# Performance work log

Hardware: AMD Instinct MI355X
Metric: run time of the kernel (lower is better)

Reference implementation:

```python
import jax, jax.numpy as jnp
import numpy as np

H = 16  # num_heads
LN_EPS = 1e-5


def _layernorm(x):
    # parameter-free LayerNorm over last dim (the source module creates no LN params)
    mu = jnp.mean(x, axis=-1, keepdims=True)
    var = jnp.var(x, axis=-1, keepdims=True)
    return (x - mu) / jnp.sqrt(var + LN_EPS)


def setup_inputs() -> dict:
    key = jax.random.key(0)
    B, L, D = 8, 1024, 1024
    ks = jax.random.split(key, 12)
    s = 1.0 / np.sqrt(D)
    s4 = 1.0 / np.sqrt(4 * D)
    return {
        "x": jax.random.normal(ks[0], (B, L, D), dtype=jnp.float32),
        "Wq": jax.random.normal(ks[1], (D, D), dtype=jnp.float32) * s,
        "bq": jnp.zeros((D,), dtype=jnp.float32),
        "Wk": jax.random.normal(ks[2], (D, D), dtype=jnp.float32) * s,
        "bk": jnp.zeros((D,), dtype=jnp.float32),
        "Wv": jax.random.normal(ks[3], (D, D), dtype=jnp.float32) * s,
        "bv": jnp.zeros((D,), dtype=jnp.float32),
        "W1": jax.random.normal(ks[4], (D, 4 * D), dtype=jnp.float32) * s,
        "b1": jnp.zeros((4 * D,), dtype=jnp.float32),
        "W2": jax.random.normal(ks[5], (4 * D, D), dtype=jnp.float32) * s4,
        "b2": jnp.zeros((D,), dtype=jnp.float32),
    }


def reference(x, Wq, bq, Wk, bk, Wv, bv, W1, b1, W2, b2):
    B, L, D = x.shape
    Dh = D // H

    def split(t):  # [B,L,D] -> [B,H,L,Dh]
        return t.reshape(B, L, H, Dh).transpose(0, 2, 1, 3)

    q = split(x @ Wq + bq)
    k = split(x @ Wk + bk)
    v = split(x @ Wv + bv)

    # naive full-score attention, materializes [B,H,L,L]
    score = jnp.einsum("bhld,bhmd->bhlm", q, k) / jnp.sqrt(jnp.float32(Dh))
    attn = jax.nn.softmax(score, axis=-1)
    out = jnp.einsum("bhlm,bhmd->bhld", attn, v)
    out = out.transpose(0, 2, 1, 3).reshape(B, L, D)  # concat heads

    x = _layernorm(x + out)  # dropout = identity (eval)
    ffn = jax.nn.gelu(x @ W1 + b1, approximate=False) @ W2 + b2
    x = _layernorm(x + ffn)
    return x
```

## Files before the change

### kernel.cpp

```cpp
#include <hip/hip_runtime.h>

typedef unsigned short u16;
typedef __attribute__((ext_vector_type(8))) short bf16x8;
typedef __attribute__((ext_vector_type(4))) float f32x4;

#define MFMA16(a, b, c) __builtin_amdgcn_mfma_f32_16x16x32_bf16(a, b, c, 0, 0, 0)

__device__ __forceinline__ float b2f(u16 u) {
    unsigned int x = ((unsigned int)u) << 16;
    return __builtin_bit_cast(float, x);
}
__device__ __forceinline__ u16 f2b(float f) {
    unsigned int u = __builtin_bit_cast(unsigned int, f);
    u = u + 0x7fffu + ((u >> 16) & 1u);
    return (u16)(u >> 16);
}
__device__ __forceinline__ float gelu_f(float x) {
    return 0.5f * x * (1.0f + erff(x * 0.70710678118654752f));
}
__device__ __forceinline__ void gload_lds16(const u16* g, u16* lds) {
    __builtin_amdgcn_global_load_lds(
        (const __attribute__((address_space(1))) unsigned int*)g,
        (__attribute__((address_space(3))) unsigned int*)lds, 16, 0, 0);
}

__global__ __launch_bounds__(256) void cvt_f2b_kernel(
    const float* __restrict__ in, u16* __restrict__ out, int n)
{
    const int i = (blockIdx.x * 256 + threadIdx.x) * 4;
    if (i >= n) return;
    float4 v = *(const float4*)&in[i];
    ushort4 o;
    o.x = f2b(v.x); o.y = f2b(v.y); o.z = f2b(v.z); o.w = f2b(v.w);
    *(ushort4*)&out[i] = o;
}

__global__ __launch_bounds__(256) void transpose_cvt(
    const float* __restrict__ in, u16* __restrict__ out, int R, int C)
{
    __shared__ u16 tile[64][65];
    const int t = threadIdx.x;
    const int r0 = blockIdx.y * 64, c0 = blockIdx.x * 64;
    const int tr = t >> 4, tc = (t & 15) * 4;
#pragma unroll
    for (int p = 0; p < 4; p++) {
        const int rr = tr + p * 16;
        float4 v = *(const float4*)&in[(size_t)(r0 + rr) * C + c0 + tc];
        tile[rr][tc + 0] = f2b(v.x); tile[rr][tc + 1] = f2b(v.y);
        tile[rr][tc + 2] = f2b(v.z); tile[rr][tc + 3] = f2b(v.w);
    }
    __syncthreads();
#pragma unroll
    for (int p = 0; p < 4; p++) {
        const int cc = tr + p * 16;
        ushort4 v;
        v.x = tile[tc + 0][cc]; v.y = tile[tc + 1][cc];
        v.z = tile[tc + 2][cc]; v.w = tile[tc + 3][cc];
        *(ushort4*)&out[(size_t)(c0 + cc) * R + r0 + tc] = v;
    }
}

template <int EPI>
__global__ __launch_bounds__(256, 2) void gemm_bt(
    const u16* __restrict__ A, const u16* __restrict__ Bt,
    const float* __restrict__ bias, u16* __restrict__ C,
    int M, int N, int K)
{
    __shared__ __attribute__((aligned(16))) u16 sA[2][128 * 32];
    __shared__ __attribute__((aligned(16))) u16 sB[2][128 * 32];
    const int t = threadIdx.x;
    const int lane = t & 63, w = t >> 6;
    const int g = lane >> 4, r = lane & 15;
    const int wr = w >> 1, wc = w & 1;
    const int m0 = blockIdx.y * 128, n0 = blockIdx.x * 128;
    const int arow0 = t >> 2;
    const int ake = (t & 3) * 8;
    const int ldsb = w * 512;

    const f32x4 fz = {0.f, 0.f, 0.f, 0.f};
    f32x4 acc[4][4];
#pragma unroll
    for (int i = 0; i < 4; i++)
#pragma unroll
        for (int j = 0; j < 4; j++) acc[i][j] = fz;

#pragma unroll
    for (int it = 0; it < 2; ++it) {
        gload_lds16(&A[(size_t)(m0 + arow0 + it * 64) * K + ake], &sA[0][ldsb + it * 2048]);
        gload_lds16(&Bt[(size_t)(n0 + arow0 + it * 64) * K + ake], &sB[0][ldsb + it * 2048]);
    }
    __syncthreads();

    const int nk = K >> 5;
    for (int kt = 0; kt < nk; ++kt) {
        const int buf = kt & 1;
        if (kt + 1 < nk) {
            const int k0 = (kt + 1) << 5;
#pragma unroll
            for (int it = 0; it < 2; ++it) {
                gload_lds16(&A[(size_t)(m0 + arow0 + it * 64) * K + k0 + ake], &sA[buf ^ 1][ldsb + it * 2048]);
                gload_lds16(&Bt[(size_t)(n0 + arow0 + it * 64) * K + k0 + ake], &sB[buf ^ 1][ldsb + it * 2048]);
            }
        }
        bf16x8 af[4], bfr[4];
#pragma unroll
        for (int i = 0; i < 4; i++)
            af[i] = *(const bf16x8*)&sA[buf][(wr * 64 + i * 16 + r) * 32 + g * 8];
#pragma unroll
        for (int j = 0; j < 4; j++)
            bfr[j] = *(const bf16x8*)&sB[buf][(wc * 64 + j * 16 + r) * 32 + g * 8];
#pragma unroll
        for (int i = 0; i < 4; i++)
#pragma unroll
            for (int j = 0; j < 4; j++)
                acc[i][j] = MFMA16(af[i], bfr[j], acc[i][j]);
        __syncthreads();
    }

#pragma unroll
    for (int i = 0; i < 4; i++) {
#pragma unroll
        for (int j = 0; j < 4; j++) {
            const int col = n0 + wc * 64 + j * 16 + r;
            const float bs = bias[col];
            const int row0 = m0 + wr * 64 + i * 16 + g * 4;
            if (EPI == 2) {
                const int brow = row0 >> 10;
                const int l = row0 & 1023;
                const int vrow = ((brow << 4) + (col >> 6)) * 64 + (col & 63);
                ushort4 pk;
                pk.x = f2b(acc[i][j][0] + bs);
                pk.y = f2b(acc[i][j][1] + bs);
                pk.z = f2b(acc[i][j][2] + bs);
                pk.w = f2b(acc[i][j][3] + bs);
                *(ushort4*)&C[(size_t)vrow * 1024 + l] = pk;
            } else {
#pragma unroll
                for (int rg = 0; rg < 4; ++rg) {
                    float v = acc[i][j][rg] + bs;
                    if (EPI == 1) v = gelu_f(v);
                    C[(size_t)(row0 + rg) * N + col] = f2b(v);
                }
            }
        }
    }
}

__global__ __launch_bounds__(256, 2) void attn_fwd(
    const u16* __restrict__ Q, const u16* __restrict__ Kb,
    const u16* __restrict__ Vt, u16* __restrict__ O)
{
    __shared__ __attribute__((aligned(16))) u16 sK[2][64 * 64];
    __shared__ __attribute__((aligned(16))) u16 sV[2][64 * 64];
    __shared__ __attribute__((aligned(16))) u16 sP[4][32 * 72];
    const int t = threadIdx.x;
    const int lane = t & 63, w = t >> 6;
    const int g = lane >> 4, r = lane & 15;
    const int bh = blockIdx.y;
    const int b = bh >> 4, h = bh & 15;
    const int q0 = blockIdx.x * 128;
    const size_t tokbase = (size_t)b << 10;
    const float SC = 0.125f * 1.44269504f;

    bf16x8 qf[2][2];
#pragma unroll
    for (int i = 0; i < 2; i++)
#pragma unroll
        for (int c = 0; c < 2; c++)
            qf[i][c] = *(const bf16x8*)&Q[((tokbase + q0 + w * 32 + i * 16 + r) << 10) + h * 64 + c * 32 + g * 8];

    const f32x4 fz = {0.f, 0.f, 0.f, 0.f};
    f32x4 acc[2][4];
    float lrow[2][4];
#pragma unroll
    for (int i = 0; i < 2; i++) {
#pragma unroll
        for (int j = 0; j < 4; j++) acc[i][j] = fz;
#pragma unroll
        for (int rg = 0; rg < 4; rg++) lrow[i][rg] = 0.f;
    }

    const int srow0 = t >> 3;
    const int skesw = ((t & 7) ^ ((t >> 3) & 7)) * 8;
    const int ldsb = w * 512;
    auto stageKV = [&](int kt, int bufsel) {
#pragma unroll
        for (int it = 0; it < 2; ++it) {
            const int row = srow0 + it * 32;
            gload_lds16(&Kb[((tokbase + kt * 64 + row) << 10) + h * 64 + skesw], &sK[bufsel][ldsb + it * 2048]);
            gload_lds16(&Vt[(((size_t)bh * 64 + row) << 10) + kt * 64 + skesw], &sV[bufsel][ldsb + it * 2048]);
        }
    };

    stageKV(0, 0);
    __syncthreads();

    for (int kt = 0; kt < 16; ++kt) {
        const int buf = kt & 1;
        if (kt < 15) stageKV(kt + 1, buf ^ 1);

        f32x4 s[2][4];
#pragma unroll
        for (int i = 0; i < 2; i++)
#pragma unroll
            for (int j = 0; j < 4; j++) s[i][j] = fz;
#pragma unroll
        for (int c = 0; c < 2; c++) {
            bf16x8 kf[4];
#pragma unroll
            for (int j = 0; j < 4; j++)
                kf[j] = *(const bf16x8*)&sK[buf][(j * 16 + r) * 64 + (((c * 4 + g) ^ (r & 7)) * 8)];
#pragma unroll
            for (int i = 0; i < 2; i++)
#pragma unroll
                for (int j = 0; j < 4; j++)
                    s[i][j] = MFMA16(qf[i][c], kf[j], s[i][j]);
        }

#pragma unroll
        for (int i = 0; i < 2; i++) {
#pragma unroll
            for (int rg = 0; rg < 4; rg++) {
                float p0 = __builtin_amdgcn_exp2f(s[i][0][rg] * SC);
                float p1 = __builtin_amdgcn_exp2f(s[i][1][rg] * SC);
                float p2 = __builtin_amdgcn_exp2f(s[i][2][rg] * SC);
                float p3 = __builtin_amdgcn_exp2f(s[i][3][rg] * SC);
                lrow[i][rg] += (p0 + p1) + (p2 + p3);
                const int prow = (i * 16 + g * 4 + rg) * 72;
                sP[w][prow + 0 * 16 + r] = f2b(p0);
                sP[w][prow + 1 * 16 + r] = f2b(p1);
                sP[w][prow + 2 * 16 + r] = f2b(p2);
                sP[w][prow + 3 * 16 + r] = f2b(p3);
            }
        }

#pragma unroll
        for (int c = 0; c < 2; c++) {
            bf16x8 pa[2], vb[4];
#pragma unroll
            for (int i = 0; i < 2; i++)
                pa[i] = *(const bf16x8*)&sP[w][(i * 16 + r) * 72 + c * 32 + g * 8];
#pragma unroll
            for (int j = 0; j < 4; j++)
                vb[j] = *(const bf16x8*)&sV[buf][(j * 16 + r) * 64 + (((c * 4 + g) ^ (r & 7)) * 8)];
#pragma unroll
            for (int i = 0; i < 2; i++)
#pragma unroll
                for (int j = 0; j < 4; j++)
                    acc[i][j] = MFMA16(pa[i], vb[j], acc[i][j]);
        }
        __syncthreads();
    }

#pragma unroll
    for (int i = 0; i < 2; i++)
#pragma unroll
        for (int rg = 0; rg < 4; rg++) {
            float l = lrow[i][rg];
            l += __shfl_xor(l, 1);
            l += __shfl_xor(l, 2);
            l += __shfl_xor(l, 4);
            l += __shfl_xor(l, 8);
            lrow[i][rg] = 1.0f / l;
        }
#pragma unroll
    for (int i = 0; i < 2; i++)
#pragma unroll
        for (int j = 0; j < 4; j++)
#pragma unroll
            for (int rg = 0; rg < 4; rg++) {
                const size_t row = tokbase + q0 + w * 32 + i * 16 + g * 4 + rg;
                const int col = h * 64 + j * 16 + r;
                O[(row << 10) + col] = f2b(acc[i][j][rg] * lrow[i][rg]);
            }
}

template <int FP32OUT>
__global__ __launch_bounds__(256) void resln(
    const u16* __restrict__ a, const u16* __restrict__ bsrc, void* __restrict__ optr)
{
    const int row = blockIdx.x, t = threadIdx.x;
    const size_t base = (size_t)row << 10;
    ushort4 va = *(const ushort4*)&a[base + t * 4];
    ushort4 vb = *(const ushort4*)&bsrc[base + t * 4];
    float v0 = b2f(va.x) + b2f(vb.x);
    float v1 = b2f(va.y) + b2f(vb.y);
    float v2 = b2f(va.z) + b2f(vb.z);
    float v3 = b2f(va.w) + b2f(vb.w);
    float s = v0 + v1 + v2 + v3;
    float ss = v0 * v0 + v1 * v1 + v2 * v2 + v3 * v3;
#pragma unroll
    for (int m = 1; m < 64; m <<= 1) { s += __shfl_xor(s, m); ss += __shfl_xor(ss, m); }
    __shared__ float rs[4], rq[4];
    const int w = t >> 6;
    if ((t & 63) == 0) { rs[w] = s; rq[w] = ss; }
    __syncthreads();
    s = rs[0] + rs[1] + rs[2] + rs[3];
    ss = rq[0] + rq[1] + rq[2] + rq[3];
    const float mu = s * (1.0f / 1024.0f);
    const float var = ss * (1.0f / 1024.0f) - mu * mu;
    const float ri = rsqrtf(var + 1e-5f);
    if (FP32OUT) {
        float4 vo;
        vo.x = (v0 - mu) * ri; vo.y = (v1 - mu) * ri;
        vo.z = (v2 - mu) * ri; vo.w = (v3 - mu) * ri;
        *(float4*)&((float*)optr)[base + t * 4] = vo;
    } else {
        ushort4 vo;
        vo.x = f2b((v0 - mu) * ri); vo.y = f2b((v1 - mu) * ri);
        vo.z = f2b((v2 - mu) * ri); vo.w = f2b((v3 - mu) * ri);
        *(ushort4*)&((u16*)optr)[base + t * 4] = vo;
    }
}

extern "C" void kernel_launch(void* const* d_in, const int* in_sizes, int n_in,
                              void* d_out, int out_size, void* d_ws, size_t ws_size,
                              hipStream_t stream)
{
    (void)in_sizes; (void)n_in; (void)out_size; (void)ws_size;
    const float* x  = (const float*)d_in[0];
    const float* Wq = (const float*)d_in[1];
    const float* bq = (const float*)d_in[2];
    const float* Wk = (const float*)d_in[3];
    const float* bk = (const float*)d_in[4];
    const float* Wv = (const float*)d_in[5];
    const float* bv = (const float*)d_in[6];
    const float* W1 = (const float*)d_in[7];
    const float* b1 = (const float*)d_in[8];
    const float* W2 = (const float*)d_in[9];
    const float* b2 = (const float*)d_in[10];
    float* out = (float*)d_out;
    char* ws = (char*)d_ws;
    const size_t MB = 1u << 20;
    u16* Qb  = (u16*)(ws + 0 * MB);
    u16* Kbf = (u16*)(ws + 16 * MB);
    u16* Vt  = (u16*)(ws + 32 * MB);
    u16* Ob  = (u16*)(ws + 48 * MB);
    u16* xb  = (u16*)(ws + 64 * MB);
    u16* X1  = (u16*)(ws + 80 * MB);
    u16* W1T = (u16*)(ws + 96 * MB);
    u16* WqT = (u16*)(ws + 104 * MB);
    u16* WkT = (u16*)(ws + 106 * MB);
    u16* WvT = (u16*)(ws + 108 * MB);
    u16* W2T = (u16*)(ws + 104 * MB);
    u16* Hb  = (u16*)(ws + 0 * MB);
    u16* H2  = (u16*)(ws + 64 * MB);

    dim3 blk(256);
    cvt_f2b_kernel<<<dim3(8192), blk, 0, stream>>>(x, xb, 8192 * 1024);
    transpose_cvt<<<dim3(16, 16), blk, 0, stream>>>(Wq, WqT, 1024, 1024);
    transpose_cvt<<<dim3(16, 16), blk, 0, stream>>>(Wk, WkT, 1024, 1024);
    transpose_cvt<<<dim3(16, 16), blk, 0, stream>>>(Wv, WvT, 1024, 1024);
    transpose_cvt<<<dim3(64, 16), blk, 0, stream>>>(W1, W1T, 1024, 4096);

    gemm_bt<0><<<dim3(8, 64), blk, 0, stream>>>(xb, WqT, bq, Qb, 8192, 1024, 1024);
    gemm_bt<0><<<dim3(8, 64), blk, 0, stream>>>(xb, WkT, bk, Kbf, 8192, 1024, 1024);
    gemm_bt<2><<<dim3(8, 64), blk, 0, stream>>>(xb, WvT, bv, Vt, 8192, 1024, 1024);

    transpose_cvt<<<dim3(16, 64), blk, 0, stream>>>(W2, W2T, 4096, 1024);

    attn_fwd<<<dim3(8, 128), blk, 0, stream>>>(Qb, Kbf, Vt, Ob);

    resln<0><<<dim3(8192), blk, 0, stream>>>(xb, Ob, X1);

    gemm_bt<1><<<dim3(32, 64), blk, 0, stream>>>(X1, W1T, b1, Hb, 8192, 4096, 1024);
    gemm_bt<0><<<dim3(8, 64), blk, 0, stream>>>(Hb, W2T, b2, H2, 8192, 1024, 4096);

    resln<1><<<dim3(8192), blk, 0, stream>>>(X1, H2, out);
}
```

Before: 411.5 us.

## Fuse Q/K/V projections into one GEMM and add XCD-aware block swizzle

Concatenates the transposed Wq, Wk and Wv into one contiguous weight buffer and replaces three separate projection launches with a single 24x64-block GEMM. Its epilogue picks the bias and output buffer by column range and keeps the transposed V layout. All GEMMs now remap block indices so that consecutive tiles land on the same XCD, aiming for better L2 reuse of A and B tiles across the chiplets. The goals are fewer launches, better wave fill, and reuse of the x tile across Q/K/V, at the cost of a slightly more complex epilogue with a per-block branch.

```diff
diff --git a/kernel.cpp b/kernel.cpp
--- a/kernel.cpp
+++ b/kernel.cpp
@@ -22,6 +22,16 @@
     __builtin_amdgcn_global_load_lds(
         (const __attribute__((address_space(1))) unsigned int*)g,
         (__attribute__((address_space(3))) unsigned int*)lds, 16, 0, 0);
+}
+__device__ __forceinline__ void swz_block(int& mb, int& nb) {
+    const int NX = gridDim.x;
+    const int nwg = NX * gridDim.y;
+    const int wg = blockIdx.y * NX + blockIdx.x;
+    const int q = nwg >> 3, rmd = nwg & 7;
+    const int xcd = wg & 7, idx = wg >> 3;
+    const int swz = (xcd < rmd ? xcd * (q + 1) : rmd * (q + 1) + (xcd - rmd) * q) + idx;
+    mb = swz / NX;
+    nb = swz - mb * NX;
 }
 
 __global__ __launch_bounds__(256) void cvt_f2b_kernel(
@@ -72,7 +82,9 @@
     const int lane = t & 63, w = t >> 6;
     const int g = lane >> 4, r = lane & 15;
     const int wr = w >> 1, wc = w & 1;
-    const int m0 = blockIdx.y * 128, n0 = blockIdx.x * 128;
+    int mb, nb;
+    swz_block(mb, nb);
+    const int m0 = mb * 128, n0 = nb * 128;
     const int arow0 = t >> 2;
     const int ake = (t & 3) * 8;
     const int ldsb = w * 512;
@@ -124,23 +136,101 @@
             const int col = n0 + wc * 64 + j * 16 + r;
             const float bs = bias[col];
             const int row0 = m0 + wr * 64 + i * 16 + g * 4;
-            if (EPI == 2) {
+#pragma unroll
+            for (int rg = 0; rg < 4; ++rg) {
+                float v = acc[i][j][rg] + bs;
+                if (EPI == 1) v = gelu_f(v);
+                C[(size_t)(row0 + rg) * N + col] = f2b(v);
+            }
+        }
+    }
+}
+
+__global__ __launch_bounds__(256, 2) void gemm_qkv(
+    const u16* __restrict__ A, const u16* __restrict__ Bt,
+    const float* __restrict__ bq, const float* __restrict__ bk,
+    const float* __restrict__ bv,
+    u16* __restrict__ Qo, u16* __restrict__ Ko, u16* __restrict__ Vt,
+    int M, int K)
+{
+    __shared__ __attribute__((aligned(16))) u16 sA[2][128 * 32];
+    __shared__ __attribute__((aligned(16))) u16 sB[2][128 * 32];
+    const int t = threadIdx.x;
+    const int lane = t & 63, w = t >> 6;
+    const int g = lane >> 4, r = lane & 15;
+    const int wr = w >> 1, wc = w & 1;
+    int mb, nb;
+    swz_block(mb, nb);
+    const int m0 = mb * 128, n0 = nb * 128;
+    const int arow0 = t >> 2;
+    const int ake = (t & 3) * 8;
+    const int ldsb = w * 512;
+
+    const f32x4 fz = {0.f, 0.f, 0.f, 0.f};
+    f32x4 acc[4][4];
+#pragma unroll
+    for (int i = 0; i < 4; i++)
+#pragma unroll
+        for (int j = 0; j < 4; j++) acc[i][j] = fz;
+
+#pragma unroll
+    for (int it = 0; it < 2; ++it) {
+        gload_lds16(&A[(size_t)(m0 + arow0 + it * 64) * K + ake], &sA[0][ldsb + it * 2048]);
+        gload_lds16(&Bt[(size_t)(n0 + arow0 + it * 64) * K + ake], &sB[0][ldsb + it * 2048]);
+    }
+    __syncthreads();
+
+    const int nk = K >> 5;
+    for (int kt = 0; kt < nk; ++kt) {
+        const int buf = kt & 1;
+        if (kt + 1 < nk) {
+            const int k0 = (kt + 1) << 5;
+#pragma unroll
+            for (int it = 0; it < 2; ++it) {
+                gload_lds16(&A[(size_t)(m0 + arow0 + it * 64) * K + k0 + ake], &sA[buf ^ 1][ldsb + it * 2048]);
+                gload_lds16(&Bt[(size_t)(n0 + arow0 + it * 64) * K + k0 + ake], &sB[buf ^ 1][ldsb + it * 2048]);
+            }
+        }
+        bf16x8 af[4], bfr[4];
+#pragma unroll
+        for (int i = 0; i < 4; i++)
+            af[i] = *(const bf16x8*)&sA[buf][(wr * 64 + i * 16 + r) * 32 + g * 8];
+#pragma unroll
+        for (int j = 0; j < 4; j++)
+            bfr[j] = *(const bf16x8*)&sB[buf][(wc * 64 + j * 16 + r) * 32 + g * 8];
+#pragma unroll
+        for (int i = 0; i < 4; i++)
+#pragma unroll
+            for (int j = 0; j < 4; j++)
+                acc[i][j] = MFMA16(af[i], bfr[j], acc[i][j]);
+        __syncthreads();
+    }
+
+    const int sel = n0 >> 10;
+    const float* bias = (sel == 0) ? bq : (sel == 1) ? bk : bv;
+#pragma unroll
+    for (int i = 0; i < 4; i++) {
+#pragma unroll
+        for (int j = 0; j < 4; j++) {
+            const int col = n0 + wc * 64 + j * 16 + r;
+            const int c1 = col & 1023;
+            const float bs = bias[c1];
+            const int row0 = m0 + wr * 64 + i * 16 + g * 4;
+            if (sel < 2) {
+                u16* C = sel ? Ko : Qo;
+#pragma unroll
+                for (int rg = 0; rg < 4; ++rg)
+                    C[(size_t)(row0 + rg) * 1024 + c1] = f2b(acc[i][j][rg] + bs);
+            } else {
                 const int brow = row0 >> 10;
                 const int l = row0 & 1023;
-                const int vrow = ((brow << 4) + (col >> 6)) * 64 + (col & 63);
+                const int vrow = ((brow << 4) + (c1 >> 6)) * 64 + (c1 & 63);
                 ushort4 pk;
                 pk.x = f2b(acc[i][j][0] + bs);
                 pk.y = f2b(acc[i][j][1] + bs);
                 pk.z = f2b(acc[i][j][2] + bs);
                 pk.w = f2b(acc[i][j][3] + bs);
-                *(ushort4*)&C[(size_t)vrow * 1024 + l] = pk;
-            } else {
-#pragma unroll
-                for (int rg = 0; rg < 4; ++rg) {
-                    float v = acc[i][j][rg] + bs;
-                    if (EPI == 1) v = gelu_f(v);
-                    C[(size_t)(row0 + rg) * N + col] = f2b(v);
-                }
+                *(ushort4*)&Vt[(size_t)vrow * 1024 + l] = pk;
             }
         }
     }
@@ -332,30 +422,27 @@
     float* out = (float*)d_out;
     char* ws = (char*)d_ws;
     const size_t MB = 1u << 20;
-    u16* Qb  = (u16*)(ws + 0 * MB);
-    u16* Kbf = (u16*)(ws + 16 * MB);
-    u16* Vt  = (u16*)(ws + 32 * MB);
-    u16* Ob  = (u16*)(ws + 48 * MB);
-    u16* xb  = (u16*)(ws + 64 * MB);
-    u16* X1  = (u16*)(ws + 80 * MB);
-    u16* W1T = (u16*)(ws + 96 * MB);
-    u16* WqT = (u16*)(ws + 104 * MB);
-    u16* WkT = (u16*)(ws + 106 * MB);
-    u16* WvT = (u16*)(ws + 108 * MB);
-    u16* W2T = (u16*)(ws + 104 * MB);
-    u16* Hb  = (u16*)(ws + 0 * MB);
-    u16* H2  = (u16*)(ws + 64 * MB);
+    u16* Qb     = (u16*)(ws + 0 * MB);
+    u16* Kbf    = (u16*)(ws + 16 * MB);
+    u16* Vt     = (u16*)(ws + 32 * MB);
+    u16* Ob     = (u16*)(ws + 48 * MB);
+    u16* xb     = (u16*)(ws + 64 * MB);
+    u16* X1     = (u16*)(ws + 80 * MB);
+    u16* W1T    = (u16*)(ws + 96 * MB);
+    u16* WqkvT  = (u16*)(ws + 104 * MB);
+    u16* W2T    = (u16*)(ws + 104 * MB);
+    u16* Hb     = (u16*)(ws + 0 * MB);
+    u16* H2     = (u16*)(ws + 64 * MB);
 
     dim3 blk(256);
     cvt_f2b_kernel<<<dim3(8192), blk, 0, stream>>>(x, xb, 8192 * 1024);
-    transpose_cvt<<<dim3(16, 16), blk, 0, stream>>>(Wq, WqT, 1024, 1024);
-    transpose_cvt<<<dim3(16, 16), blk, 0, stream>>>(Wk, WkT, 1024, 1024);
-    transpose_cvt<<<dim3(16, 16), blk, 0, stream>>>(Wv, WvT, 1024, 1024);
+    transpose_cvt<<<dim3(16, 16), blk, 0, stream>>>(Wq, WqkvT, 1024, 1024);
+    transpose_cvt<<<dim3(16, 16), blk, 0, stream>>>(Wk, WqkvT + 1024 * 1024, 1024, 1024);
+    transpose_cvt<<<dim3(16, 16), blk, 0, stream>>>(Wv, WqkvT + 2048 * 1024, 1024, 1024);
     transpose_cvt<<<dim3(64, 16), blk, 0, stream>>>(W1, W1T, 1024, 4096);
 
-    gemm_bt<0><<<dim3(8, 64), blk, 0, stream>>>(xb, WqT, bq, Qb, 8192, 1024, 1024);
-    gemm_bt<0><<<dim3(8, 64), blk, 0, stream>>>(xb, WkT, bk, Kbf, 8192, 1024, 1024);
-    gemm_bt<2><<<dim3(8, 64), blk, 0, stream>>>(xb, WvT, bv, Vt, 8192, 1024, 1024);
+    gemm_qkv<<<dim3(24, 64), blk, 0, stream>>>(xb, WqkvT, bq, bk, bv,
+                                               Qb, Kbf, Vt, 8192, 1024);
 
     transpose_cvt<<<dim3(16, 64), blk, 0, stream>>>(W2, W2T, 4096, 1024);
 
```

Result: faster. 383.9 us (-6.7%).
